# Optimization experiments

Hardware: AMD Instinct MI355X
Metric: run time of the kernel (lower is better)

## Reference

```python
import jax, jax.numpy as jnp
import numpy as np

B, S, D = 1, 2048, 2048
H, KV, HD = 32, 8, 64  # heads, kv heads, head_dim
THETA = 10000.0


def rot(x):
    # torch: cat(-x[..., d/2:], x[..., :d/2])
    f, s = jnp.split(x, 2, axis=-1)
    return jnp.concatenate((-s, f), axis=-1)


def setup_inputs() -> dict:
    key = jax.random.key(0)
    k0, k1, k2, k3, k4 = jax.random.split(key, 5)
    x = jax.random.normal(k0, (B, S, D), jnp.float32)
    Wq = jax.random.normal(k1, (H * HD, D), jnp.float32) * 0.02
    Wk = jax.random.normal(k2, (KV * HD, D), jnp.float32) * 0.02
    Wv = jax.random.normal(k3, (KV * HD, D), jnp.float32) * 0.02
    Wo = jax.random.normal(k4, (D, H * HD), jnp.float32) * 0.02
    inv_freq = 1.0 / (THETA ** (jnp.arange(0, HD, 2, dtype=jnp.float32) / HD))
    return {"x": x, "Wq": Wq, "Wk": Wk, "Wv": Wv, "Wo": Wo, "inv_freq": inv_freq}


def reference(x, Wq, Wk, Wv, Wo, inv_freq):
    bsz, seqlen, _ = x.shape
    q = (x @ Wq.T).reshape(bsz, seqlen, H, HD).transpose(0, 2, 1, 3)   # [B,H,S,hd]
    k = (x @ Wk.T).reshape(bsz, seqlen, KV, HD).transpose(0, 2, 1, 3)  # [B,KV,S,hd]
    v = (x @ Wv.T).reshape(bsz, seqlen, KV, HD).transpose(0, 2, 1, 3)

    # RoPE cos/sin (computed under no_grad in torch)
    pos = jnp.arange(seqlen, dtype=jnp.float32)
    freqs = pos[:, None] * inv_freq[None, :]                # [S, hd/2]
    emb = jnp.concatenate((freqs, freqs), axis=-1)          # [S, hd]
    cos = jnp.cos(emb)[None, None]                          # [1,1,S,hd]
    sin = jnp.sin(emb)[None, None]
    q = q * cos + rot(q) * sin
    k = k * cos + rot(k) * sin

    # GQA: group query heads per kv head instead of repeat_interleaving kv
    G = H // KV
    qg = q.reshape(bsz, KV, G, seqlen, HD)
    scores = jnp.einsum('bkgsd,bktd->bkgst', qg, k) / jnp.sqrt(jnp.float32(HD))
    mask = jnp.triu(jnp.full((seqlen, seqlen), -jnp.inf, jnp.float32), 1)
    attn = jax.nn.softmax(scores + mask, axis=-1)
    out = jnp.einsum('bkgst,bktd->bkgsd', attn, v)          # [B,KV,G,S,hd]
    out = out.reshape(bsz, H, seqlen, HD).transpose(0, 2, 1, 3).reshape(bsz, seqlen, H * HD)
    return out @ Wo.T
```

## Files before the change

### kernel.cpp

```cpp
#include <hip/hip_runtime.h>
#include <hip/hip_bf16.h>
#include <math.h>

#define S_LEN 2048
#define D_MODEL 2048
#define N_H 32
#define N_KV 8
#define HD 64

typedef __attribute__((ext_vector_type(8))) short short8;
typedef __attribute__((ext_vector_type(4))) float floatx4;
typedef unsigned short u16;
typedef unsigned int u32;

#define QSCALE 0.18033688011112042f

#if defined(__has_builtin)
#if __has_builtin(__builtin_amdgcn_exp2f)
#define EXP2(x) __builtin_amdgcn_exp2f(x)
#else
#define EXP2(x) __expf(0.6931471805599453f * (x))
#endif
#else
#define EXP2(x) __expf(0.6931471805599453f * (x))
#endif

__device__ __forceinline__ u16 f2bf(float f) {
    union { float f; u32 u; } v; v.f = f;
    u32 r = v.u + 0x7fffu + ((v.u >> 16) & 1u);
    return (u16)(r >> 16);
}

__device__ __forceinline__ void gload16(const void* gp, void* lp) {
    __builtin_amdgcn_global_load_lds(
        (const __attribute__((address_space(1))) unsigned int*)gp,
        (__attribute__((address_space(3))) unsigned int*)lp,
        16, 0, 0);
}

__global__ __launch_bounds__(256) void cast_all(const float* __restrict__ x,
                                                const float* __restrict__ Wq,
                                                const float* __restrict__ Wk,
                                                const float* __restrict__ Wv,
                                                const float* __restrict__ Wo,
                                                u16* __restrict__ xb,
                                                u16* __restrict__ wqkv,
                                                u16* __restrict__ wob) {
    const int i = (blockIdx.x * 256 + threadIdx.x) * 4;
    const int row = i >> 11;
    const int col = i & 2047;
    const float* src;
    u16* dst;
    if (row < 2048)      { src = x  + (size_t)row * 2048 + col;          dst = xb + i; }
    else if (row < 4096) { src = Wq + (size_t)(row - 2048) * 2048 + col; dst = wqkv + (i - 2048 * 2048); }
    else if (row < 4608) { src = Wk + (size_t)(row - 4096) * 2048 + col; dst = wqkv + (i - 2048 * 2048); }
    else if (row < 5120) { src = Wv + (size_t)(row - 4608) * 2048 + col; dst = wqkv + (i - 2048 * 2048); }
    else                 { src = Wo + (size_t)(row - 5120) * 2048 + col; dst = wob + (i - 5120 * 2048); }
    const float4 v = *(const float4*)src;
    ushort4 o;
    o.x = f2bf(v.x); o.y = f2bf(v.y); o.z = f2bf(v.z); o.w = f2bf(v.w);
    *(ushort4*)dst = o;
}

__global__ __launch_bounds__(256) void gemm_qkv(const u16* __restrict__ A,
                                                const u16* __restrict__ B,
                                                u16* __restrict__ Qh,
                                                u16* __restrict__ Kh,
                                                u16* __restrict__ Vt,
                                                const float* __restrict__ inv_freq,
                                                int K) {
    __shared__ u16 As[2][64 * 32];
    __shared__ u16 Bs[2][128 * 32];
    const int tid  = threadIdx.x;
    const int w    = tid >> 6;
    const int lane = tid & 63;
    const int lr   = lane & 15;
    const int quad = lane >> 4;
    const int bm = blockIdx.x * 64, bn = blockIdx.y * 128;
    const int wm = (w & 1) * 32, wn = (w >> 1) * 64;

    const int srow = tid >> 2;
    const int sch  = (tid & 3) * 8;
    const u16* Ag = A + (size_t)(bm + srow) * K + sch;
    const u16* Bg = B + (size_t)(bn + srow) * K + sch;
    const int loff = srow * 32 + sch;
    const size_t gstride = (size_t)64 * K;

    floatx4 acc[2][4];
#pragma unroll
    for (int i = 0; i < 2; ++i)
#pragma unroll
        for (int j = 0; j < 4; ++j) acc[i][j] = floatx4{0.f, 0.f, 0.f, 0.f};

    gload16(Ag, &As[0][loff]);
    gload16(Bg, &Bs[0][loff]);
    gload16(Bg + gstride, &Bs[0][loff + 64 * 32]);
    __syncthreads();

    for (int k0 = 0; k0 < K; k0 += 32) {
        const int cur = (k0 >> 5) & 1;
        if (k0 + 32 < K) {
            gload16(Ag + k0 + 32, &As[cur ^ 1][loff]);
            gload16(Bg + k0 + 32, &Bs[cur ^ 1][loff]);
            gload16(Bg + gstride + k0 + 32, &Bs[cur ^ 1][loff + 64 * 32]);
        }
        short8 af[2], bf[4];
#pragma unroll
        for (int t = 0; t < 2; ++t)
            af[t] = *(const short8*)&As[cur][(wm + t * 16 + lr) * 32 + quad * 8];
#pragma unroll
        for (int t = 0; t < 4; ++t)
            bf[t] = *(const short8*)&Bs[cur][(wn + t * 16 + lr) * 32 + quad * 8];
#pragma unroll
        for (int im = 0; im < 2; ++im)
#pragma unroll
            for (int in = 0; in < 4; ++in)
                acc[im][in] = __builtin_amdgcn_mfma_f32_16x16x32_bf16(
                    af[im], bf[in], acc[im][in], 0, 0, 0);
        __syncthreads();
    }

    const int c0 = bn + wn;
    if (bn < 2048) {
        const int h = c0 >> 6;
#pragma unroll
        for (int p = 0; p < 2; ++p) {
            const int d = p * 16 + lr;
            const float fr = inv_freq[d];
#pragma unroll
            for (int im = 0; im < 2; ++im)
#pragma unroll
                for (int r = 0; r < 4; ++r) {
                    const int s = bm + wm + im * 16 + quad * 4 + r;
                    float sn, cs;
                    sincosf((float)s * fr, &sn, &cs);
                    const float xl = acc[im][p][r], xh = acc[im][p + 2][r];
                    u16* qrow = Qh + ((size_t)h * S_LEN + s) * HD;
                    qrow[d]      = f2bf((xl * cs - xh * sn) * QSCALE);
                    qrow[d + 32] = f2bf((xh * cs + xl * sn) * QSCALE);
                }
        }
    } else if (bn < 2560) {
        const int kv = (c0 - 2048) >> 6;
#pragma unroll
        for (int p = 0; p < 2; ++p) {
            const int d = p * 16 + lr;
            const float fr = inv_freq[d];
#pragma unroll
            for (int im = 0; im < 2; ++im)
#pragma unroll
                for (int r = 0; r < 4; ++r) {
                    const int s = bm + wm + im * 16 + quad * 4 + r;
                    float sn, cs;
                    sincosf((float)s * fr, &sn, &cs);
                    const float xl = acc[im][p][r], xh = acc[im][p + 2][r];
                    u16* krow = Kh + ((size_t)kv * S_LEN + s) * HD;
                    krow[d]      = f2bf(xl * cs - xh * sn);
                    krow[d + 32] = f2bf(xh * cs + xl * sn);
                }
        }
    } else {
        const int kv = (c0 - 2560) >> 6;
#pragma unroll
        for (int im = 0; im < 2; ++im)
#pragma unroll
            for (int in = 0; in < 4; ++in) {
                const int dfull = in * 16 + lr;
                const int s0 = bm + wm + im * 16 + quad * 4;
                ushort4 o;
                o.x = f2bf(acc[im][in][0]); o.y = f2bf(acc[im][in][1]);
                o.z = f2bf(acc[im][in][2]); o.w = f2bf(acc[im][in][3]);
                *(ushort4*)&Vt[((size_t)kv * HD + dfull) * S_LEN + s0] = o;
            }
    }
}

__global__ __launch_bounds__(256) void gemm_out(const u16* __restrict__ A,
                                                const u16* __restrict__ B,
                                                float* __restrict__ Cf,
                                                int N, int K) {
    __shared__ u16 As[2][64 * 64];
    __shared__ u16 Bs[2][64 * 64];
    const int tid  = threadIdx.x;
    const int w    = tid >> 6;
    const int lane = tid & 63;
    const int lr   = lane & 15;
    const int quad = lane >> 4;
    const int bm = blockIdx.x * 64, bn = blockIdx.y * 64;
    const int wm = w * 16;

    const int srow = tid >> 3;
    const int sch  = tid & 7;

    floatx4 acc[4];
#pragma unroll
    for (int j = 0; j < 4; ++j) acc[j] = floatx4{0.f, 0.f, 0.f, 0.f};

#pragma unroll
    for (int j = 0; j < 2; ++j) {
        const int r = j * 32 + srow;
        gload16(A + (size_t)(bm + r) * K + ((sch ^ (r & 7)) * 8),
                &As[0][r * 64 + sch * 8]);
        gload16(B + (size_t)(bn + r) * K + ((sch ^ (r & 7)) * 8),
                &Bs[0][r * 64 + sch * 8]);
    }
    __syncthreads();

    for (int k0 = 0; k0 < K; k0 += 64) {
        const int cur = (k0 >> 6) & 1;
        if (k0 + 64 < K) {
            const int nb = cur ^ 1;
#pragma unroll
            for (int j = 0; j < 2; ++j) {
                const int r = j * 32 + srow;
                gload16(A + (size_t)(bm + r) * K + k0 + 64 + ((sch ^ (r & 7)) * 8),
                        &As[nb][r * 64 + sch * 8]);
                gload16(B + (size_t)(bn + r) * K + k0 + 64 + ((sch ^ (r & 7)) * 8),
                        &Bs[nb][r * 64 + sch * 8]);
            }
        }
#pragma unroll
        for (int kk = 0; kk < 2; ++kk) {
            short8 af, bf[4];
            {
                const int row = wm + lr;
                const int c   = kk * 4 + quad;
                af = *(const short8*)&As[cur][row * 64 + ((c ^ (row & 7)) * 8)];
            }
#pragma unroll
            for (int in = 0; in < 4; ++in) {
                const int row = in * 16 + lr;
                const int c   = kk * 4 + quad;
                bf[in] = *(const short8*)&Bs[cur][row * 64 + ((c ^ (row & 7)) * 8)];
            }
#pragma unroll
            for (int in = 0; in < 4; ++in)
                acc[in] = __builtin_amdgcn_mfma_f32_16x16x32_bf16(
                    af, bf[in], acc[in], 0, 0, 0);
        }
        __syncthreads();
    }

#pragma unroll
    for (int in = 0; in < 4; ++in) {
        const int row0 = bm + wm + quad * 4;
        const int col  = bn + in * 16 + lr;
#pragma unroll
        for (int r = 0; r < 4; ++r)
            Cf[(size_t)(row0 + r) * N + col] = acc[in][r];
    }
}

__global__ __launch_bounds__(256) void attn_mfma(const u16* __restrict__ Qh,
                                                 const u16* __restrict__ Kh,
                                                 const u16* __restrict__ Vt,
                                                 u16* __restrict__ AO) {
    __shared__ u16 QPs[64 * 64];
    __shared__ u16 Ks[2][64 * 64];
    __shared__ u16 Vs[2][64 * 64];

    const int bid = blockIdx.x;
    const int h   = bid & 31;
    const int qb  = 31 - (bid >> 5);
    const int kv  = h >> 2;
    const int tid  = threadIdx.x;
    const int w    = tid >> 6;
    const int lr   = tid & 15;
    const int quad = (tid >> 4) & 3;
    const int grow = tid >> 3;
    const int gp   = tid & 7;

    const u16* Qg = Qh + ((size_t)h * S_LEN + (size_t)qb * 64) * HD;
    const u16* Kg = Kh + (size_t)kv * S_LEN * HD;
    const u16* Vg = Vt + (size_t)kv * HD * S_LEN;

#pragma unroll
    for (int j = 0; j < 2; ++j) {
        const int r = j * 32 + grow;
        gload16(Qg + (size_t)r * HD + ((gp ^ (r & 7)) * 8), QPs + r * 64 + gp * 8);
        gload16(Kg + (size_t)r * HD + ((gp ^ (r & 7)) * 8), &Ks[0][r * 64 + gp * 8]);
        gload16(Vg + (size_t)r * S_LEN + ((gp ^ (r & 7)) * 8), &Vs[0][r * 64 + gp * 8]);
    }
    __syncthreads();

    const int wq0 = qb * 64 + w * 16;

    short8 qf[2];
#pragma unroll
    for (int kh = 0; kh < 2; ++kh) {
        const int row = w * 16 + lr;
        const int c   = kh * 4 + quad;
        qf[kh] = *(const short8*)&QPs[row * 64 + ((c ^ (row & 7)) * 8)];
    }

    const int q1  = quad >> 1;
    const int lr7 = lr & 7;
    const int pwbase = (w * 16 + lr) * 64 + (quad & 1) * 4;

    float l_lane = 0.f;
    floatx4 oacc[4];
#pragma unroll
    for (int dn = 0; dn < 4; ++dn) oacc[dn] = floatx4{0.f, 0.f, 0.f, 0.f};

    const int qg = 0;
    (void)qg;

    for (int kt = 0; kt <= qb; ++kt) {
        const int buf = kt & 1;
        if (kt < qb) {
            const int nb = buf ^ 1;
#pragma unroll
            for (int j = 0; j < 2; ++j) {
                const int r = j * 32 + grow;
                gload16(Kg + (size_t)((kt + 1) * 64 + r) * HD + ((gp ^ (r & 7)) * 8),
                        &Ks[nb][r * 64 + gp * 8]);
                gload16(Vg + (size_t)r * S_LEN + (kt + 1) * 64 + ((gp ^ (r & 7)) * 8),
                        &Vs[nb][r * 64 + gp * 8]);
            }
        }
        if (64 * kt <= wq0 + 15) {
            floatx4 st[4];
#pragma unroll
            for (int in = 0; in < 4; ++in) st[in] = floatx4{0.f, 0.f, 0.f, 0.f};
#pragma unroll
            for (int in = 0; in < 4; ++in)
#pragma unroll
                for (int kh = 0; kh < 2; ++kh) {
                    const int row = in * 16 + lr;
                    const int c   = kh * 4 + quad;
                    const short8 kf = *(const short8*)
                        &Ks[buf][row * 64 + ((c ^ (row & 7)) * 8)];
                    st[in] = __builtin_amdgcn_mfma_f32_16x16x32_bf16(
                        kf, qf[kh], st[in], 0, 0, 0);
                }

            const bool need_mask = (kt * 64 + 63) > wq0;
            const int qglob = wq0 + lr;
#pragma unroll
            for (int in = 0; in < 4; ++in)
#pragma unroll
                for (int r = 0; r < 4; ++r) {
                    float s = st[in][r];
                    if (need_mask) {
                        const int kg = kt * 64 + in * 16 + quad * 4 + r;
                        if (kg > qglob) s = -1e30f;
                    }
                    const float p = EXP2(s);
                    st[in][r] = p;
                    l_lane += p;
                }

#pragma unroll
            for (int in = 0; in < 4; ++in) {
                const int chunk = (((in * 2 + q1) ^ lr7) << 3);
                float2 lo2; lo2.x = st[in][0]; lo2.y = st[in][1];
                float2 hi2; hi2.x = st[in][2]; hi2.y = st[in][3];
                __hip_bfloat162 blo = __float22bfloat162_rn(lo2);
                __hip_bfloat162 bhi = __float22bfloat162_rn(hi2);
                *(u32*)&QPs[pwbase + chunk]     = *(u32*)&blo;
                *(u32*)&QPs[pwbase + chunk + 2] = *(u32*)&bhi;
            }

#pragma unroll
            for (int kc = 0; kc < 2; ++kc) {
                const int prow = w * 16 + lr;
                const short8 pf = *(const short8*)
                    &QPs[prow * 64 + (((kc * 4 + quad) ^ (prow & 7)) * 8)];
#pragma unroll
                for (int dn = 0; dn < 4; ++dn) {
                    const int vrow = dn * 16 + lr;
                    const int c    = kc * 4 + quad;
                    const short8 vf = *(const short8*)
                        &Vs[buf][vrow * 64 + ((c ^ (vrow & 7)) * 8)];
                    oacc[dn] = __builtin_amdgcn_mfma_f32_16x16x32_bf16(
                        pf, vf, oacc[dn], 0, 0, 0);
                }
            }
        }
        __syncthreads();
    }

    float lv = l_lane;
    lv += __shfl_xor(lv, 16);
    lv += __shfl_xor(lv, 32);
#pragma unroll
    for (int r = 0; r < 4; ++r) {
        const float inv = 1.f / __shfl(lv, quad * 4 + r);
        const size_t row = (size_t)(wq0 + quad * 4 + r);
#pragma unroll
        for (int dn = 0; dn < 4; ++dn)
            AO[row * D_MODEL + h * 64 + dn * 16 + lr] =
                f2bf(oacc[dn][r] * inv);
    }
}

extern "C" void kernel_launch(void* const* d_in, const int* in_sizes, int n_in,
                              void* d_out, int out_size, void* d_ws, size_t ws_size,
                              hipStream_t stream) {
    const float* x        = (const float*)d_in[0];
    const float* Wq       = (const float*)d_in[1];
    const float* Wk       = (const float*)d_in[2];
    const float* Wv       = (const float*)d_in[3];
    const float* Wo       = (const float*)d_in[4];
    const float* inv_freq = (const float*)d_in[5];
    float* out = (float*)d_out;

    const size_t ME = 1 << 20;
    u16* xb   = (u16*)d_ws;
    u16* wqkv = xb   + 4 * ME;
    u16* wob  = wqkv + 6 * ME;
    u16* qhb  = wob  + 4 * ME;
    u16* khb  = qhb  + 4 * ME;
    u16* vtb  = khb  + 1 * ME;
    u16* aob  = vtb  + 1 * ME;

    const dim3 b256(256);

    cast_all<<<14336, b256, 0, stream>>>(x, Wq, Wk, Wv, Wo, xb, wqkv, wob);

    gemm_qkv<<<dim3(32, 24), b256, 0, stream>>>(
        xb, wqkv, qhb, khb, vtb, inv_freq, D_MODEL);

    attn_mfma<<<dim3(1024), b256, 0, stream>>>(qhb, khb, vtb, aob);

    gemm_out<<<dim3(32, 32), b256, 0, stream>>>(
        aob, wob, out, D_MODEL, D_MODEL);
}
```

Measured before the change: 208.2 us.

## Precompute RoPE cos/sin table in cast kernel and use grid-stride casting

Adds a cos/sin table for RoPE, built inside the cast kernel, so the QKV GEMM epilogue reads precomputed values instead of calling sincosf per element. The cast kernel also switches from 14336 blocks to 2048 blocks that each handle 7 chunks. The goal is to take transcendental math off the GEMM epilogue and cut block launch overhead in the cast. In exchange it adds a 512KB table write and read, and gathers from the table in the epilogue.

```diff
diff --git a/kernel.cpp b/kernel.cpp
--- a/kernel.cpp
+++ b/kernel.cpp
@@ -43,23 +43,36 @@
                                                 const float* __restrict__ Wk,
                                                 const float* __restrict__ Wv,
                                                 const float* __restrict__ Wo,
+                                                const float* __restrict__ inv_freq,
                                                 u16* __restrict__ xb,
                                                 u16* __restrict__ wqkv,
-                                                u16* __restrict__ wob) {
-    const int i = (blockIdx.x * 256 + threadIdx.x) * 4;
-    const int row = i >> 11;
-    const int col = i & 2047;
-    const float* src;
-    u16* dst;
-    if (row < 2048)      { src = x  + (size_t)row * 2048 + col;          dst = xb + i; }
-    else if (row < 4096) { src = Wq + (size_t)(row - 2048) * 2048 + col; dst = wqkv + (i - 2048 * 2048); }
-    else if (row < 4608) { src = Wk + (size_t)(row - 4096) * 2048 + col; dst = wqkv + (i - 2048 * 2048); }
-    else if (row < 5120) { src = Wv + (size_t)(row - 4608) * 2048 + col; dst = wqkv + (i - 2048 * 2048); }
-    else                 { src = Wo + (size_t)(row - 5120) * 2048 + col; dst = wob + (i - 5120 * 2048); }
-    const float4 v = *(const float4*)src;
-    ushort4 o;
-    o.x = f2bf(v.x); o.y = f2bf(v.y); o.z = f2bf(v.z); o.w = f2bf(v.w);
-    *(ushort4*)dst = o;
+                                                u16* __restrict__ wob,
+                                                float2* __restrict__ tab) {
+    const int t0 = blockIdx.x * 256 + threadIdx.x;
+#pragma unroll
+    for (int j = 0; j < 7; ++j) {
+        const int c = t0 + j * 524288;
+        const int i = c * 4;
+        const int row = i >> 11;
+        const int col = i & 2047;
+        const float* src;
+        u16* dst;
+        if (row < 2048)      { src = x  + (size_t)row * 2048 + col;          dst = xb + i; }
+        else if (row < 4096) { src = Wq + (size_t)(row - 2048) * 2048 + col; dst = wqkv + (i - 2048 * 2048); }
+        else if (row < 4608) { src = Wk + (size_t)(row - 4096) * 2048 + col; dst = wqkv + (i - 2048 * 2048); }
+        else if (row < 5120) { src = Wv + (size_t)(row - 4608) * 2048 + col; dst = wqkv + (i - 2048 * 2048); }
+        else                 { src = Wo + (size_t)(row - 5120) * 2048 + col; dst = wob + (i - 5120 * 2048); }
+        const float4 v = *(const float4*)src;
+        ushort4 o;
+        o.x = f2bf(v.x); o.y = f2bf(v.y); o.z = f2bf(v.z); o.w = f2bf(v.w);
+        *(ushort4*)dst = o;
+    }
+    if (t0 < 65536) {
+        const int s = t0 >> 5, d = t0 & 31;
+        float sn, cs;
+        sincosf((float)s * inv_freq[d], &sn, &cs);
+        tab[t0] = make_float2(cs, sn);
+    }
 }
 
 __global__ __launch_bounds__(256) void gemm_qkv(const u16* __restrict__ A,
@@ -67,7 +80,7 @@
                                                 u16* __restrict__ Qh,
                                                 u16* __restrict__ Kh,
                                                 u16* __restrict__ Vt,
-                                                const float* __restrict__ inv_freq,
+                                                const float2* __restrict__ tab,
                                                 int K) {
     __shared__ u16 As[2][64 * 32];
     __shared__ u16 Bs[2][128 * 32];
@@ -126,14 +139,13 @@
 #pragma unroll
         for (int p = 0; p < 2; ++p) {
             const int d = p * 16 + lr;
-            const float fr = inv_freq[d];
 #pragma unroll
             for (int im = 0; im < 2; ++im)
 #pragma unroll
                 for (int r = 0; r < 4; ++r) {
                     const int s = bm + wm + im * 16 + quad * 4 + r;
-                    float sn, cs;
-                    sincosf((float)s * fr, &sn, &cs);
+                    const float2 t = tab[s * 32 + d];
+                    const float cs = t.x, sn = t.y;
                     const float xl = acc[im][p][r], xh = acc[im][p + 2][r];
                     u16* qrow = Qh + ((size_t)h * S_LEN + s) * HD;
                     qrow[d]      = f2bf((xl * cs - xh * sn) * QSCALE);
@@ -145,14 +157,13 @@
 #pragma unroll
         for (int p = 0; p < 2; ++p) {
             const int d = p * 16 + lr;
-            const float fr = inv_freq[d];
 #pragma unroll
             for (int im = 0; im < 2; ++im)
 #pragma unroll
                 for (int r = 0; r < 4; ++r) {
                     const int s = bm + wm + im * 16 + quad * 4 + r;
-                    float sn, cs;
-                    sincosf((float)s * fr, &sn, &cs);
+                    const float2 t = tab[s * 32 + d];
+                    const float cs = t.x, sn = t.y;
                     const float xl = acc[im][p][r], xh = acc[im][p + 2][r];
                     u16* krow = Kh + ((size_t)kv * S_LEN + s) * HD;
                     krow[d]      = f2bf(xl * cs - xh * sn);
@@ -302,9 +313,6 @@
 #pragma unroll
     for (int dn = 0; dn < 4; ++dn) oacc[dn] = floatx4{0.f, 0.f, 0.f, 0.f};
 
-    const int qg = 0;
-    (void)qg;
-
     for (int kt = 0; kt <= qb; ++kt) {
         const int buf = kt & 1;
         if (kt < qb) {
@@ -413,13 +421,15 @@
     u16* khb  = qhb  + 4 * ME;
     u16* vtb  = khb  + 1 * ME;
     u16* aob  = vtb  + 1 * ME;
+    float2* cstab = (float2*)(aob + 4 * ME);
 
     const dim3 b256(256);
 
-    cast_all<<<14336, b256, 0, stream>>>(x, Wq, Wk, Wv, Wo, xb, wqkv, wob);
+    cast_all<<<2048, b256, 0, stream>>>(x, Wq, Wk, Wv, Wo, inv_freq,
+                                        xb, wqkv, wob, cstab);
 
     gemm_qkv<<<dim3(32, 24), b256, 0, stream>>>(
-        xb, wqkv, qhb, khb, vtb, inv_freq, D_MODEL);
+        xb, wqkv, qhb, khb, vtb, cstab, D_MODEL);
 
     attn_mfma<<<dim3(1024), b256, 0, stream>>>(qhb, khb, vtb, aob);
 
```

After: 208.4 us. Within noise of the previous version (+0.1%).
